# Performance work log

Hardware: AMD Instinct MI355X
Metric: run time of the kernel (lower is better)

## Reference

```python
import jax, jax.numpy as jnp
import numpy as np

B, N, K = 4, 4096, 16
D_POINTS, D_MODEL = 64, 128


def setup_inputs() -> dict:
    key = jax.random.key(0)
    ks = jax.random.split(key, 18)
    rn = lambda k, shp, s=0.05: (jax.random.normal(k, shp, jnp.float32) * s)
    return {
        "xyz": jax.random.normal(ks[0], (B, N, 3), jnp.float32),
        "features": jax.random.normal(ks[1], (B, N, D_POINTS), jnp.float32),
        # fc_delta: Linear(3,d_model) -> ReLU -> Linear(d_model,d_model)
        "Wd1": rn(ks[2], (3, D_MODEL)), "bd1": rn(ks[3], (D_MODEL,)),
        "Wd2": rn(ks[4], (D_MODEL, D_MODEL)), "bd2": rn(ks[5], (D_MODEL,)),
        # fc1: Linear(d_points, d_model)
        "Wf1": rn(ks[6], (D_POINTS, D_MODEL)), "bf1": rn(ks[7], (D_MODEL,)),
        # w_qs / w_ks / w_vs: Linear(d_model, d_model, bias=False)
        "Wq": rn(ks[8], (D_MODEL, D_MODEL)),
        "Wk": rn(ks[9], (D_MODEL, D_MODEL)),
        "Wv": rn(ks[10], (D_MODEL, D_MODEL)),
        # fc_gamma: Linear(d_model,d_model) -> ReLU -> Linear(d_model,d_model)
        "Wg1": rn(ks[11], (D_MODEL, D_MODEL)), "bg1": rn(ks[12], (D_MODEL,)),
        "Wg2": rn(ks[13], (D_MODEL, D_MODEL)), "bg2": rn(ks[14], (D_MODEL,)),
        # fc2: Linear(d_model, d_points)
        "Wo": rn(ks[15], (D_MODEL, D_POINTS)), "bo": rn(ks[16], (D_POINTS,)),
    }


def reference(xyz, features, Wd1, bd1, Wd2, bd2, Wf1, bf1, Wq, Wk, Wv,
              Wg1, bg1, Wg2, bg2, Wo, bo):
    sq = jnp.sum(xyz * xyz, axis=-1)
    d2 = sq[:, :, None] + sq[:, None, :] - 2.0 * jnp.einsum('bnd,bmd->bnm', xyz, xyz)
    # argsort()[:, :, :k] == k smallest distances (self included)
    _, knn_idx = jax.lax.top_k(-d2, K)  # [B,N,K] int32

    gather = jax.vmap(lambda a, i: a[i])  # per-batch fancy gather along point axis
    knn_xyz = gather(xyz, knn_idx)                       # [B,N,K,3]
    rel = xyz[:, :, None, :] - knn_xyz                   # [B,N,K,3]
    pos_enc = jax.nn.relu(rel @ Wd1 + bd1) @ Wd2 + bd2   # [B,N,K,D]

    shortcut = features
    f = features @ Wf1 + bf1                             # [B,N,D]
    knn_f = gather(f, knn_idx)                           # [B,N,K,D]

    q = f @ Wq                                           # [B,N,D]
    k = knn_f @ Wk                                       # [B,N,K,D]
    v = knn_f @ Wv                                       # [B,N,K,D]

    attn = q[:, :, None, :] - k + pos_enc                # [B,N,K,D]
    attn = jax.nn.relu(attn @ Wg1 + bg1) @ Wg2 + bg2
    attn = jax.nn.softmax(attn / np.sqrt(D_MODEL).astype(np.float32), axis=-2)

    res = jnp.einsum('bnkf,bnkf->bnf', attn, v + pos_enc)  # [B,N,D]
    return res @ Wo + bo + shortcut                        # [B,N,d_points]
```

## Files before the change

kernel.cpp:

```cpp
#include <hip/hip_runtime.h>
#include <hip/hip_bf16.h>

#define NPTS 4096
#define BATCH 4
#define BN (BATCH * NPTS)
#define DMODEL 128
#define DPTS 64
#define KNBR 16
#define SWS 136

typedef unsigned short u16;
typedef unsigned int u32;
typedef unsigned long long u64;
typedef short bh8 __attribute__((ext_vector_type(8)));
typedef float f32x4 __attribute__((ext_vector_type(4)));

__device__ __forceinline__ float bfu(u16 u) {
    union { u32 i; float f; } c; c.i = ((u32)u) << 16; return c.f;
}
__device__ __forceinline__ u16 f2u(float x) {
    u32 u = __float_as_uint(x);
    u32 r = u + 0x7FFFu + ((u >> 16) & 1u);
    return (u16)(r >> 16);
}
__device__ __forceinline__ u32 pack2(float a, float b) {
    return (u32)f2u(a) | ((u32)f2u(b) << 16);
}
__device__ __forceinline__ float ldr(const void* p, long i, int mode) {
    return mode == 0 ? bfu(((const u16*)p)[i]) : ((const float*)p)[i];
}
__device__ __forceinline__ void str(void* p, long i, float v, int mode) {
    if (mode == 0) ((u16*)p)[i] = f2u(v);
    else ((float*)p)[i] = v;
}
__device__ __forceinline__ int detect_mode(const void* Wq) {
    const u16* w = (const u16*)Wq;
    int lane = threadIdx.x & 63;
    int tot = 0;
#pragma unroll
    for (int r = 0; r < 4; ++r) {
        unsigned e = (w[lane + r * 64] >> 7) & 0xFFu;
        bool wild = (e >= 132u) || (e > 0u && e <= 90u);
        tot += (int)__popcll(__ballot(wild));
    }
    return tot > 32 ? 1 : 0;
}

__global__ __launch_bounds__(256) void prep_kernel(
    const void* __restrict__ Wd2, const void* __restrict__ Wg1, const void* __restrict__ Wg2,
    const void* __restrict__ Wo, const void* __restrict__ Wq, const void* __restrict__ Wk,
    const void* __restrict__ Wv, const void* __restrict__ Wf1,
    u16* __restrict__ WdT2, u16* __restrict__ WgT1, u16* __restrict__ WgT2,
    u16* __restrict__ WoT, u16* __restrict__ WqT, u16* __restrict__ WkT,
    u16* __restrict__ WvT, u16* __restrict__ WfT) {
    int mode = detect_mode(Wq);
    int gid = blockIdx.x * 256 + threadIdx.x;
    if (gid < 6 * 16384) {
        int m = gid >> 14, o = gid & 16383;
        int n = o >> 7, i = o & 127;
        const void* W = (m == 0) ? Wd2 : (m == 1) ? Wg1 : (m == 2) ? Wg2
                      : (m == 3) ? Wq  : (m == 4) ? Wk  : Wv;
        u16* D = (m == 0) ? WdT2 : (m == 1) ? WgT1 : (m == 2) ? WgT2
               : (m == 3) ? WqT  : (m == 4) ? WkT  : WvT;
        D[o] = f2u(ldr(W, (long)i * 128 + n, mode));
    } else if (gid < 6 * 16384 + 8192) {
        int o = gid - 6 * 16384;
        int n = o >> 6, k2 = o & 63;
        WfT[o] = f2u(ldr(Wf1, (long)k2 * 128 + n, mode));
    } else if (gid < 6 * 16384 + 16384) {
        int o2 = gid - 6 * 16384 - 8192;
        int col = o2 >> 7, i = o2 & 127;
        WoT[o2] = f2u(ldr(Wo, (long)i * 64 + col, mode));
    }
}

__global__ __launch_bounds__(256) void qkv_kernel(
    const void* __restrict__ feat, const void* __restrict__ bf1v, const void* __restrict__ WqRaw,
    const u16* __restrict__ WfT, const u16* __restrict__ WqT,
    const u16* __restrict__ WkT, const u16* __restrict__ WvT,
    u16* __restrict__ qw, u16* __restrict__ kfw, u16* __restrict__ vfw) {
    int mode = detect_mode(WqRaw);
    __shared__ __align__(16) u16 sFeat[64 * 72];
    __shared__ __align__(16) u16 sF[64 * SWS];
    const int t = threadIdx.x;
    const int p0 = blockIdx.x * 64;
    const int lane = t & 63, w = t >> 6;
    const int rg = (w & 1) * 32, cg = (w >> 1) * 64;
    const int lm = lane & 15, lq = lane >> 4;

    for (int i = t; i < 512; i += 256) {
        int r = i >> 3, c8 = i & 7;
        u16 tmp[8];
        if (mode == 0) {
            *(uint4*)tmp = *((const uint4*)feat + (long)(p0 + r) * 8 + c8);
        } else {
            const float* fp = (const float*)feat + (long)(p0 + r) * 64 + c8 * 8;
#pragma unroll
            for (int u = 0; u < 8; ++u) tmp[u] = f2u(fp[u]);
        }
        *(uint4*)(sFeat + r * 72 + c8 * 8) = *(uint4*)tmp;
    }
    __syncthreads();

    {
        f32x4 acc[2][4];
#pragma unroll
        for (int rt = 0; rt < 2; ++rt)
#pragma unroll
            for (int ct = 0; ct < 4; ++ct) { acc[rt][ct][0]=0.f; acc[rt][ct][1]=0.f; acc[rt][ct][2]=0.f; acc[rt][ct][3]=0.f; }
#pragma unroll
        for (int kk = 0; kk < 2; ++kk) {
            const int ko = kk * 32 + lq * 8;
            bh8 a0 = *(const bh8*)(sFeat + (rg + lm) * 72 + ko);
            bh8 a1 = *(const bh8*)(sFeat + (rg + 16 + lm) * 72 + ko);
            bh8 bq[4];
#pragma unroll
            for (int ct = 0; ct < 4; ++ct)
                bq[ct] = *(const bh8*)(WfT + (long)(cg + ct * 16 + lm) * 64 + ko);
#pragma unroll
            for (int ct = 0; ct < 4; ++ct) {
                acc[0][ct] = __builtin_amdgcn_mfma_f32_16x16x32_bf16(a0, bq[ct], acc[0][ct], 0, 0, 0);
                acc[1][ct] = __builtin_amdgcn_mfma_f32_16x16x32_bf16(a1, bq[ct], acc[1][ct], 0, 0, 0);
            }
        }
#pragma unroll
        for (int rt = 0; rt < 2; ++rt)
#pragma unroll
            for (int ct = 0; ct < 4; ++ct) {
                const int col = cg + ct * 16 + lm;
                const float bj = ldr(bf1v, col, mode);
#pragma unroll
                for (int r4 = 0; r4 < 4; ++r4) {
                    int row = rg + rt * 16 + lq * 4 + r4;
                    u32 u = (u32)f2u(acc[rt][ct][r4] + bj);
                    u32 o = __shfl_xor(u, 1);
                    if ((lane & 1) == 0)
                        *(u32*)(sF + row * SWS + col) = u | (o << 16);
                }
            }
    }
    __syncthreads();

    const u16* Ws[3] = {WqT, WkT, WvT};
    u16* Os[3] = {qw, kfw, vfw};
#pragma unroll 1
    for (int m = 0; m < 3; ++m) {
        f32x4 acc[2][4];
#pragma unroll
        for (int rt = 0; rt < 2; ++rt)
#pragma unroll
            for (int ct = 0; ct < 4; ++ct) { acc[rt][ct][0]=0.f; acc[rt][ct][1]=0.f; acc[rt][ct][2]=0.f; acc[rt][ct][3]=0.f; }
#pragma unroll
        for (int kk = 0; kk < 4; ++kk) {
            const int ko = kk * 32 + lq * 8;
            bh8 a0 = *(const bh8*)(sF + (rg + lm) * SWS + ko);
            bh8 a1 = *(const bh8*)(sF + (rg + 16 + lm) * SWS + ko);
            bh8 bq[4];
#pragma unroll
            for (int ct = 0; ct < 4; ++ct)
                bq[ct] = *(const bh8*)(Ws[m] + (long)(cg + ct * 16 + lm) * 128 + ko);
#pragma unroll
            for (int ct = 0; ct < 4; ++ct) {
                acc[0][ct] = __builtin_amdgcn_mfma_f32_16x16x32_bf16(a0, bq[ct], acc[0][ct], 0, 0, 0);
                acc[1][ct] = __builtin_amdgcn_mfma_f32_16x16x32_bf16(a1, bq[ct], acc[1][ct], 0, 0, 0);
            }
        }
#pragma unroll
        for (int rt = 0; rt < 2; ++rt)
#pragma unroll
            for (int ct = 0; ct < 4; ++ct) {
                const int col = cg + ct * 16 + lm;
#pragma unroll
                for (int r4 = 0; r4 < 4; ++r4) {
                    int row = rg + rt * 16 + lq * 4 + r4;
                    u32 u = (u32)f2u(acc[rt][ct][r4]);
                    u32 o = __shfl_xor(u, 1);
                    if ((lane & 1) == 0)
                        *(u32*)(Os[m] + (long)(p0 + row) * DMODEL + col) = u | (o << 16);
                }
            }
    }
}

__device__ __forceinline__ void mfma4(const u16* sIn, const u16* __restrict__ Bg,
                                      const float* bias, bool dorelu, bool inplace,
                                      u16* sOut, int t) {
    const int lane = t & 63, w = t >> 6;
    const int rg = (w & 1) * 32, cg = (w >> 1) * 64;
    const int lm = lane & 15, lq = lane >> 4;
    f32x4 acc[2][4];
#pragma unroll
    for (int rt = 0; rt < 2; ++rt)
#pragma unroll
        for (int ct = 0; ct < 4; ++ct) { acc[rt][ct][0]=0.f; acc[rt][ct][1]=0.f; acc[rt][ct][2]=0.f; acc[rt][ct][3]=0.f; }
#pragma unroll
    for (int kk = 0; kk < 4; ++kk) {
        const int ko = kk * 32 + lq * 8;
        bh8 a0 = *(const bh8*)(sIn + (rg + lm) * SWS + ko);
        bh8 a1 = *(const bh8*)(sIn + (rg + 16 + lm) * SWS + ko);
        bh8 bq[4];
#pragma unroll
        for (int ct = 0; ct < 4; ++ct)
            bq[ct] = *(const bh8*)(Bg + (long)(cg + ct * 16 + lm) * 128 + ko);
#pragma unroll
        for (int ct = 0; ct < 4; ++ct) {
            acc[0][ct] = __builtin_amdgcn_mfma_f32_16x16x32_bf16(a0, bq[ct], acc[0][ct], 0, 0, 0);
            acc[1][ct] = __builtin_amdgcn_mfma_f32_16x16x32_bf16(a1, bq[ct], acc[1][ct], 0, 0, 0);
        }
    }
    if (inplace) __syncthreads();
#pragma unroll
    for (int rt = 0; rt < 2; ++rt)
#pragma unroll
        for (int ct = 0; ct < 4; ++ct) {
            const int col = cg + ct * 16 + lm;
            const float bj = bias[col];
#pragma unroll
            for (int r4 = 0; r4 < 4; ++r4) {
                int row = rg + rt * 16 + lq * 4 + r4;
                float v = acc[rt][ct][r4] + bj;
                if (dorelu) v = fmaxf(v, 0.f);
                u32 u = (u32)f2u(v);
                u32 o = __shfl_xor(u, 1);
                if ((lane & 1) == 0)
                    *(u32*)(sOut + row * SWS + col) = u | (o << 16);
            }
        }
}

#define ATT_SA 0
#define ATT_SPE 17408
#define ATT_SREL 34816
#define ATT_SBIAS 35840
#define ATT_SQ 37376
#define SMEM_BYTES 38400

__global__ __launch_bounds__(256, 4) void fused_kernel(
    const void* __restrict__ xyz, const void* __restrict__ feat,
    const void* __restrict__ Wd1, const void* __restrict__ bd1, const void* __restrict__ bd2,
    const void* __restrict__ bg1, const void* __restrict__ bg2, const void* __restrict__ bo,
    const void* __restrict__ WqRaw,
    const u16* __restrict__ WdT2, const u16* __restrict__ WgT1, const u16* __restrict__ WgT2,
    const u16* __restrict__ WoT,
    const u16* __restrict__ qw, const u16* __restrict__ kfw, const u16* __restrict__ vfw,
    void* __restrict__ out) {
    int mode = detect_mode(WqRaw);
    __shared__ __align__(16) char smem[SMEM_BYTES];
    __shared__ int sIdx[64];
    u16* sXyz = (u16*)smem;
    u16* sA   = (u16*)(smem + ATT_SA);
    u16* sPE  = (u16*)(smem + ATT_SPE);
    float (*sRel)[4] = (float(*)[4])(smem + ATT_SREL);
    float* sBias = (float*)(smem + ATT_SBIAS);
    u16* sQ   = (u16*)(smem + ATT_SQ);

    const int t = threadIdx.x, lane = t & 63, w = t >> 6;
    const int lm = lane & 15, lq = lane >> 4;
    const int p0 = blockIdx.x * 4;
    const long bbase = (long)(p0 >> 12) * NPTS;
    const long xb = bbase * 3;

    for (int m = t; m < NPTS; m += 256) {
        float gx = ldr(xyz, xb + m * 3 + 0, mode);
        float gy = ldr(xyz, xb + m * 3 + 1, mode);
        float gz = ldr(xyz, xb + m * 3 + 2, mode);
        uint2 pk;
        pk.x = (u32)f2u(gx) | ((u32)f2u(gy) << 16);
        pk.y = (u32)f2u(gz);
        *(uint2*)(sXyz + m * 4) = pk;
    }
    __syncthreads();

    {
        const int pl = (p0 & (NPTS - 1)) + w;
        uint2 qv = *(const uint2*)(sXyz + pl * 4);
        const float px = __uint_as_float(qv.x << 16);
        const float py = __uint_as_float(qv.x & 0xFFFF0000u);
        const float pz = __uint_as_float(qv.y << 16);

        u64 kv;
        {
            uint2 c = *(const uint2*)(sXyz + lane * 4);
            float cx = __uint_as_float(c.x << 16);
            float cy = __uint_as_float(c.x & 0xFFFF0000u);
            float cz = __uint_as_float(c.y << 16);
            float key = fmaf(px * cx + py * cy + pz * cz, -2.f,
                             cx * cx + cy * cy + cz * cz);
            u32 uk = __float_as_uint(key);
            uk ^= (u32)((int)uk >> 31) | 0x80000000u;
            kv = ((u64)uk << 32) | (u32)lane;
#pragma unroll
            for (int k = 2; k <= 64; k <<= 1) {
#pragma unroll
                for (int j = k >> 1; j > 0; j >>= 1) {
                    u64 other = __shfl_xor(kv, j);
                    bool keepMin = ((lane & j) == 0) == ((lane & k) == 0);
                    bool smaller = kv < other;
                    kv = (keepMin == smaller) ? kv : other;
                }
            }
        }
        u32 Tu = __builtin_amdgcn_readlane((u32)(kv >> 32), 15);

        uint2 cd0 = *(const uint2*)(sXyz + (64 + lane) * 4);
        uint2 cd1 = *(const uint2*)(sXyz + (128 + lane) * 4);
#pragma unroll 1
        for (int it = 0; it < 32; ++it) {
            const int base = 64 + it * 128;
            uint2 c0 = cd0, c1 = cd1;
            if (it < 31) {
                int n0 = base + 128 + lane;
                int n1 = n0 + 64 > 4095 ? 4095 : n0 + 64;
                cd0 = *(const uint2*)(sXyz + n0 * 4);
                cd1 = *(const uint2*)(sXyz + n1 * 4);
            }
            float cx0 = __uint_as_float(c0.x << 16);
            float cy0 = __uint_as_float(c0.x & 0xFFFF0000u);
            float cz0 = __uint_as_float(c0.y << 16);
            float cx1 = __uint_as_float(c1.x << 16);
            float cy1 = __uint_as_float(c1.x & 0xFFFF0000u);
            float cz1 = __uint_as_float(c1.y << 16);
            float k0 = fmaf(px * cx0 + py * cy0 + pz * cz0, -2.f,
                            cx0 * cx0 + cy0 * cy0 + cz0 * cz0);
            float k1 = fmaf(px * cx1 + py * cy1 + pz * cz1, -2.f,
                            cx1 * cx1 + cy1 * cy1 + cz1 * cz1);
            u32 u0 = __float_as_uint(k0); u0 ^= (u32)((int)u0 >> 31) | 0x80000000u;
            u32 u1 = __float_as_uint(k1); u1 ^= (u32)((int)u1 >> 31) | 0x80000000u;
            if (it == 31) u1 = 0xFFFFFFFFu;
            u32 umin = (u0 < u1) ? u0 : u1;
            unsigned long long mask = __ballot(umin < Tu);
            while (mask) {
                int l = __ffsll(mask) - 1;
                mask &= mask - 1;
                u32 a0 = __builtin_amdgcn_readlane(u0, l);
                u32 a1 = __builtin_amdgcn_readlane(u1, l);
                if (a0 < Tu) {
                    u64 cand = ((u64)a0 << 32) | (u32)(base + l);
                    u64 prev = __shfl_up(kv, 1);
                    if (lane == 0) prev = 0;
                    kv = (prev > cand) ? prev : ((kv > cand) ? cand : kv);
                    Tu = __builtin_amdgcn_readlane((u32)(kv >> 32), 15);
                }
                if (a1 < Tu) {
                    u64 cand = ((u64)a1 << 32) | (u32)(base + 64 + l);
                    u64 prev = __shfl_up(kv, 1);
                    if (lane == 0) prev = 0;
                    kv = (prev > cand) ? prev : ((kv > cand) ? cand : kv);
                    Tu = __builtin_amdgcn_readlane((u32)(kv >> 32), 15);
                }
            }
        }
        if (lane < 16) sIdx[w * 16 + lane] = (int)(u32)kv;
    }
    __syncthreads();

    for (int i = t; i < 384; i += 256) {
        const void* b = (i < 128) ? bd2 : (i < 256) ? bg1 : bg2;
        sBias[i] = ldr(b, i & 127, mode);
    }
    ((u32*)sQ)[t] = ((const u32*)(qw + (long)p0 * DMODEL))[t];
    const int ch = 2 * lane;
    const float wd0a = ldr(Wd1, ch, mode),       wd0b = ldr(Wd1, ch + 1, mode);
    const float wd1a = ldr(Wd1, 128 + ch, mode), wd1b = ldr(Wd1, 128 + ch + 1, mode);
    const float wd2a = ldr(Wd1, 256 + ch, mode), wd2b = ldr(Wd1, 256 + ch + 1, mode);
    const float bd1a = ldr(bd1, ch, mode),       bd1b = ldr(bd1, ch + 1, mode);
    if (t < 64) {
        int pl2 = (p0 & (NPTS - 1)) + (t >> 4);
        uint2 pv = *(const uint2*)(sXyz + pl2 * 4);
        uint2 nv = *(const uint2*)(sXyz + sIdx[t] * 4);
        sRel[t][0] = __uint_as_float(pv.x << 16)          - __uint_as_float(nv.x << 16);
        sRel[t][1] = __uint_as_float(pv.x & 0xFFFF0000u)  - __uint_as_float(nv.x & 0xFFFF0000u);
        sRel[t][2] = __uint_as_float(pv.y << 16)          - __uint_as_float(nv.y << 16);
    }
    __syncthreads();

#pragma unroll
    for (int i = 0; i < 16; ++i) {
        int r = w * 16 + i;
        float4 rl = *(const float4*)sRel[r];
        float h0 = fmaxf(bd1a + rl.x * wd0a + rl.y * wd1a + rl.z * wd2a, 0.f);
        float h1 = fmaxf(bd1b + rl.x * wd0b + rl.y * wd1b + rl.z * wd2b, 0.f);
        *(u32*)(sA + r * SWS + ch) = pack2(h0, h1);
    }
    __syncthreads();
    mfma4(sA, WdT2, sBias, false, false, sPE, t);
    __syncthreads();

#pragma unroll
    for (int i = 0; i < 16; ++i) {
        int r = w * 16 + i;
        u32 kv2 = *(const u32*)(kfw + (bbase + sIdx[r]) * (long)DMODEL + ch);
        u32 qv2 = *(const u32*)(sQ + (r >> 4) * DMODEL + ch);
        u32 pe2 = *(const u32*)(sPE + r * SWS + ch);
        float a0 = bfu((u16)qv2) - bfu((u16)kv2) + bfu((u16)pe2);
        float a1 = bfu((u16)(qv2 >> 16)) - bfu((u16)(kv2 >> 16)) + bfu((u16)(pe2 >> 16));
        *(u32*)(sA + r * SWS + ch) = pack2(a0, a1);
    }
    __syncthreads();
    mfma4(sA, WgT1, sBias + 128, true, true, sA, t);
    __syncthreads();
    mfma4(sA, WgT2, sBias + 256, false, true, sA, t);
    __syncthreads();

    float res0, res1;
    {
        float mx0 = -3e38f, mx1 = -3e38f;
#pragma unroll
        for (int k = 0; k < KNBR; ++k) {
            u32 l2 = *(const u32*)(sA + (w * 16 + k) * SWS + ch);
            mx0 = fmaxf(mx0, bfu((u16)l2));
            mx1 = fmaxf(mx1, bfu((u16)(l2 >> 16)));
        }
        const float inv = 0.08838834764831845f;
        float s0 = 0.f, s1 = 0.f, r0 = 0.f, r1 = 0.f;
#pragma unroll
        for (int k = 0; k < KNBR; ++k) {
            u32 l2 = *(const u32*)(sA + (w * 16 + k) * SWS + ch);
            u32 v2 = *(const u32*)(vfw + (bbase + sIdx[w * 16 + k]) * (long)DMODEL + ch);
            u32 p2 = *(const u32*)(sPE + (w * 16 + k) * SWS + ch);
            float e0 = __expf((bfu((u16)l2) - mx0) * inv);
            float e1 = __expf((bfu((u16)(l2 >> 16)) - mx1) * inv);
            s0 += e0; s1 += e1;
            r0 += e0 * (bfu((u16)v2) + bfu((u16)p2));
            r1 += e1 * (bfu((u16)(v2 >> 16)) + bfu((u16)(p2 >> 16)));
        }
        res0 = r0 / s0; res1 = r1 / s1;
    }
    __syncthreads();
    *(u32*)(sA + w * SWS + ch) = pack2(res0, res1);
    __syncthreads();

    {
        const int col = w * 16 + lm;
        f32x4 acc = {0.f, 0.f, 0.f, 0.f};
#pragma unroll
        for (int kk = 0; kk < 4; ++kk) {
            const int ko = kk * 32 + lq * 8;
            bh8 aa = *(const bh8*)(sA + lm * SWS + ko);
            bh8 bb = *(const bh8*)(WoT + (long)col * DMODEL + ko);
            acc = __builtin_amdgcn_mfma_f32_16x16x32_bf16(aa, bb, acc, 0, 0, 0);
        }
        if (lq == 0) {
            float bov = ldr(bo, col, mode);
#pragma unroll
            for (int r4 = 0; r4 < 4; ++r4) {
                long p = p0 + r4;
                float v = acc[r4] + bov + ldr(feat, p * DPTS + col, mode);
                str(out, p * DPTS + col, v, mode);
            }
        }
    }
}

extern "C" void kernel_launch(void* const* d_in, const int* in_sizes, int n_in,
                              void* d_out, int out_size, void* d_ws, size_t ws_size,
                              hipStream_t stream) {
    (void)in_sizes; (void)n_in; (void)out_size; (void)ws_size;
    char* ws = (char*)d_ws;
    u16* qw   = (u16*)(ws + 256);
    u16* kfw  = qw + (long)BN * DMODEL;
    u16* vfw  = kfw + (long)BN * DMODEL;
    u16* WdT2 = vfw + (long)BN * DMODEL;
    u16* WgT1 = WdT2 + 16384;
    u16* WgT2 = WgT1 + 16384;
    u16* WoT  = WgT2 + 16384;
    u16* WqT  = WoT + 8192;
    u16* WkT  = WqT + 16384;
    u16* WvT  = WkT + 16384;
    u16* WfT  = WvT + 16384;

    prep_kernel<<<448, 256, 0, stream>>>(d_in[4], d_in[11], d_in[13], d_in[15],
                                         d_in[8], d_in[9], d_in[10], d_in[6],
                                         WdT2, WgT1, WgT2, WoT, WqT, WkT, WvT, WfT);
    qkv_kernel<<<BN / 64, 256, 0, stream>>>(d_in[1], d_in[7], d_in[8],
                                            WfT, WqT, WkT, WvT, qw, kfw, vfw);
    fused_kernel<<<BN / 4, 256, 0, stream>>>(d_in[0], d_in[1], d_in[2], d_in[3], d_in[5],
                                             d_in[12], d_in[14], d_in[16], d_in[8],
                                             WdT2, WgT1, WgT2, WoT,
                                             qw, kfw, vfw, d_out);
}
```

Before: 314.7 us.

## Split kNN into its own kernel reading a prepacked bf16 point cloud

Before, every fused block of 4 query points reloaded and converted all 4096 xyz points into shared memory before the kNN search. Now the prep kernel packs xyz to bf16 once, a separate knn_kernel scans that packed cloud from global/L2 and writes neighbour indices, and the fused kernel only reads those indices. The qkv kernel also spreads the Q/K/V projections across a 3-wide grid y dimension, and the mfma4 helper is inlined. This removes heavy redundant per-block staging and cuts fused-kernel LDS traffic, at the cost of one extra launch, an index round trip, and recomputing the f = features·Wf1 projection three times in qkv.

Result: faster. 303.1 us (-3.7%).

```diff
diff --git a/kernel.cpp b/kernel.cpp
--- a/kernel.cpp
+++ b/kernel.cpp
@@ -49,10 +49,10 @@
 __global__ __launch_bounds__(256) void prep_kernel(
     const void* __restrict__ Wd2, const void* __restrict__ Wg1, const void* __restrict__ Wg2,
     const void* __restrict__ Wo, const void* __restrict__ Wq, const void* __restrict__ Wk,
-    const void* __restrict__ Wv, const void* __restrict__ Wf1,
+    const void* __restrict__ Wv, const void* __restrict__ Wf1, const void* __restrict__ xyz,
     u16* __restrict__ WdT2, u16* __restrict__ WgT1, u16* __restrict__ WgT2,
     u16* __restrict__ WoT, u16* __restrict__ WqT, u16* __restrict__ WkT,
-    u16* __restrict__ WvT, u16* __restrict__ WfT) {
+    u16* __restrict__ WvT, u16* __restrict__ WfT, uint2* __restrict__ cloud) {
     int mode = detect_mode(Wq);
     int gid = blockIdx.x * 256 + threadIdx.x;
     if (gid < 6 * 16384) {
@@ -71,6 +71,15 @@
         int o2 = gid - 6 * 16384 - 8192;
         int col = o2 >> 7, i = o2 & 127;
         WoT[o2] = f2u(ldr(Wo, (long)i * 64 + col, mode));
+    } else if (gid < 6 * 16384 + 16384 + 16384) {
+        int i = gid - (6 * 16384 + 16384);
+        float gx = ldr(xyz, (long)i * 3 + 0, mode);
+        float gy = ldr(xyz, (long)i * 3 + 1, mode);
+        float gz = ldr(xyz, (long)i * 3 + 2, mode);
+        uint2 pk;
+        pk.x = (u32)f2u(gx) | ((u32)f2u(gy) << 16);
+        pk.y = (u32)f2u(gz);
+        cloud[i] = pk;
     }
 }
 
@@ -141,10 +150,10 @@
     }
     __syncthreads();
 
-    const u16* Ws[3] = {WqT, WkT, WvT};
-    u16* Os[3] = {qw, kfw, vfw};
-#pragma unroll 1
-    for (int m = 0; m < 3; ++m) {
+    {
+        const int m = blockIdx.y;
+        const u16* Wm = (m == 0) ? WqT : (m == 1) ? WkT : WvT;
+        u16* Om = (m == 0) ? qw : (m == 1) ? kfw : vfw;
         f32x4 acc[2][4];
 #pragma unroll
         for (int rt = 0; rt < 2; ++rt)
@@ -158,7 +167,7 @@
             bh8 bq[4];
 #pragma unroll
             for (int ct = 0; ct < 4; ++ct)
-                bq[ct] = *(const bh8*)(Ws[m] + (long)(cg + ct * 16 + lm) * 128 + ko);
+                bq[ct] = *(const bh8*)(Wm + (long)(cg + ct * 16 + lm) * 128 + ko);
 #pragma unroll
             for (int ct = 0; ct < 4; ++ct) {
                 acc[0][ct] = __builtin_amdgcn_mfma_f32_16x16x32_bf16(a0, bq[ct], acc[0][ct], 0, 0, 0);
@@ -176,56 +185,98 @@
                     u32 u = (u32)f2u(acc[rt][ct][r4]);
                     u32 o = __shfl_xor(u, 1);
                     if ((lane & 1) == 0)
-                        *(u32*)(Os[m] + (long)(p0 + row) * DMODEL + col) = u | (o << 16);
+                        *(u32*)(Om + (long)(p0 + row) * DMODEL + col) = u | (o << 16);
                 }
             }
     }
 }
 
-__device__ __forceinline__ void mfma4(const u16* sIn, const u16* __restrict__ Bg,
-                                      const float* bias, bool dorelu, bool inplace,
-                                      u16* sOut, int t) {
-    const int lane = t & 63, w = t >> 6;
-    const int rg = (w & 1) * 32, cg = (w >> 1) * 64;
-    const int lm = lane & 15, lq = lane >> 4;
-    f32x4 acc[2][4];
-#pragma unroll
-    for (int rt = 0; rt < 2; ++rt)
-#pragma unroll
-        for (int ct = 0; ct < 4; ++ct) { acc[rt][ct][0]=0.f; acc[rt][ct][1]=0.f; acc[rt][ct][2]=0.f; acc[rt][ct][3]=0.f; }
-#pragma unroll
-    for (int kk = 0; kk < 4; ++kk) {
-        const int ko = kk * 32 + lq * 8;
-        bh8 a0 = *(const bh8*)(sIn + (rg + lm) * SWS + ko);
-        bh8 a1 = *(const bh8*)(sIn + (rg + 16 + lm) * SWS + ko);
-        bh8 bq[4];
-#pragma unroll
-        for (int ct = 0; ct < 4; ++ct)
-            bq[ct] = *(const bh8*)(Bg + (long)(cg + ct * 16 + lm) * 128 + ko);
-#pragma unroll
-        for (int ct = 0; ct < 4; ++ct) {
-            acc[0][ct] = __builtin_amdgcn_mfma_f32_16x16x32_bf16(a0, bq[ct], acc[0][ct], 0, 0, 0);
-            acc[1][ct] = __builtin_amdgcn_mfma_f32_16x16x32_bf16(a1, bq[ct], acc[1][ct], 0, 0, 0);
-        }
-    }
-    if (inplace) __syncthreads();
-#pragma unroll
-    for (int rt = 0; rt < 2; ++rt)
-#pragma unroll
-        for (int ct = 0; ct < 4; ++ct) {
-            const int col = cg + ct * 16 + lm;
-            const float bj = bias[col];
-#pragma unroll
-            for (int r4 = 0; r4 < 4; ++r4) {
-                int row = rg + rt * 16 + lq * 4 + r4;
-                float v = acc[rt][ct][r4] + bj;
-                if (dorelu) v = fmaxf(v, 0.f);
-                u32 u = (u32)f2u(v);
-                u32 o = __shfl_xor(u, 1);
-                if ((lane & 1) == 0)
-                    *(u32*)(sOut + row * SWS + col) = u | (o << 16);
-            }
-        }
+__global__ __launch_bounds__(256) void knn_kernel(
+    const uint2* __restrict__ cloud, int* __restrict__ knnIdx) {
+    const int t = threadIdx.x, lane = t & 63, w = t >> 6;
+    const int p0 = blockIdx.x * 4;
+    const long bbase = (long)(p0 >> 12) * NPTS;
+    const uint2* cl = cloud + bbase;
+
+    const int pl = (p0 & (NPTS - 1)) + w;
+    uint2 qv = cl[pl];
+    const float px = __uint_as_float(qv.x << 16);
+    const float py = __uint_as_float(qv.x & 0xFFFF0000u);
+    const float pz = __uint_as_float(qv.y << 16);
+
+    u64 kv;
+    {
+        uint2 c = cl[lane];
+        float cx = __uint_as_float(c.x << 16);
+        float cy = __uint_as_float(c.x & 0xFFFF0000u);
+        float cz = __uint_as_float(c.y << 16);
+        float key = fmaf(px * cx + py * cy + pz * cz, -2.f,
+                         cx * cx + cy * cy + cz * cz);
+        u32 uk = __float_as_uint(key);
+        uk ^= (u32)((int)uk >> 31) | 0x80000000u;
+        kv = ((u64)uk << 32) | (u32)lane;
+#pragma unroll
+        for (int k = 2; k <= 64; k <<= 1) {
+#pragma unroll
+            for (int j = k >> 1; j > 0; j >>= 1) {
+                u64 other = __shfl_xor(kv, j);
+                bool keepMin = ((lane & j) == 0) == ((lane & k) == 0);
+                bool smaller = kv < other;
+                kv = (keepMin == smaller) ? kv : other;
+            }
+        }
+    }
+    u32 Tu = __builtin_amdgcn_readlane((u32)(kv >> 32), 15);
+
+    uint2 cd0 = cl[64 + lane];
+    uint2 cd1 = cl[128 + lane];
+#pragma unroll 1
+    for (int it = 0; it < 32; ++it) {
+        const int base = 64 + it * 128;
+        uint2 c0 = cd0, c1 = cd1;
+        if (it < 31) {
+            int n0 = base + 128 + lane;
+            int n1 = n0 + 64 > 4095 ? 4095 : n0 + 64;
+            cd0 = cl[n0];
+            cd1 = cl[n1];
+        }
+        float cx0 = __uint_as_float(c0.x << 16);
+        float cy0 = __uint_as_float(c0.x & 0xFFFF0000u);
+        float cz0 = __uint_as_float(c0.y << 16);
+        float cx1 = __uint_as_float(c1.x << 16);
+        float cy1 = __uint_as_float(c1.x & 0xFFFF0000u);
+        float cz1 = __uint_as_float(c1.y << 16);
+        float k0 = fmaf(px * cx0 + py * cy0 + pz * cz0, -2.f,
+                        cx0 * cx0 + cy0 * cy0 + cz0 * cz0);
+        float k1 = fmaf(px * cx1 + py * cy1 + pz * cz1, -2.f,
+                        cx1 * cx1 + cy1 * cy1 + cz1 * cz1);
+        u32 u0 = __float_as_uint(k0); u0 ^= (u32)((int)u0 >> 31) | 0x80000000u;
+        u32 u1 = __float_as_uint(k1); u1 ^= (u32)((int)u1 >> 31) | 0x80000000u;
+        if (it == 31) u1 = 0xFFFFFFFFu;
+        u32 umin = (u0 < u1) ? u0 : u1;
+        unsigned long long mask = __ballot(umin < Tu);
+        while (mask) {
+            int l = __ffsll(mask) - 1;
+            mask &= mask - 1;
+            u32 a0 = __builtin_amdgcn_readlane(u0, l);
+            u32 a1 = __builtin_amdgcn_readlane(u1, l);
+            if (a0 < Tu) {
+                u64 cand = ((u64)a0 << 32) | (u32)(base + l);
+                u64 prev = __shfl_up(kv, 1);
+                if (lane == 0) prev = 0;
+                kv = (prev > cand) ? prev : ((kv > cand) ? cand : kv);
+                Tu = __builtin_amdgcn_readlane((u32)(kv >> 32), 15);
+            }
+            if (a1 < Tu) {
+                u64 cand = ((u64)a1 << 32) | (u32)(base + 64 + l);
+                u64 prev = __shfl_up(kv, 1);
+                if (lane == 0) prev = 0;
+                kv = (prev > cand) ? prev : ((kv > cand) ? cand : kv);
+                Tu = __builtin_amdgcn_readlane((u32)(kv >> 32), 15);
+            }
+        }
+    }
+    if (lane < 16) knnIdx[(long)(p0 + w) * 16 + lane] = (int)(u32)kv;
 }
 
 #define ATT_SA 0
@@ -236,7 +287,8 @@
 #define SMEM_BYTES 38400
 
 __global__ __launch_bounds__(256, 4) void fused_kernel(
-    const void* __restrict__ xyz, const void* __restrict__ feat,
+    const uint2* __restrict__ cloud, const int* __restrict__ knnIdx,
+    const void* __restrict__ feat,
     const void* __restrict__ Wd1, const void* __restrict__ bd1, const void* __restrict__ bd2,
     const void* __restrict__ bg1, const void* __restrict__ bg2, const void* __restrict__ bo,
     const void* __restrict__ WqRaw,
@@ -247,7 +299,6 @@
     int mode = detect_mode(WqRaw);
     __shared__ __align__(16) char smem[SMEM_BYTES];
     __shared__ int sIdx[64];
-    u16* sXyz = (u16*)smem;
     u16* sA   = (u16*)(smem + ATT_SA);
     u16* sPE  = (u16*)(smem + ATT_SPE);
     float (*sRel)[4] = (float(*)[4])(smem + ATT_SREL);
@@ -258,101 +309,7 @@
     const int lm = lane & 15, lq = lane >> 4;
     const int p0 = blockIdx.x * 4;
     const long bbase = (long)(p0 >> 12) * NPTS;
-    const long xb = bbase * 3;
-
-    for (int m = t; m < NPTS; m += 256) {
-        float gx = ldr(xyz, xb + m * 3 + 0, mode);
-        float gy = ldr(xyz, xb + m * 3 + 1, mode);
-        float gz = ldr(xyz, xb + m * 3 + 2, mode);
-        uint2 pk;
-        pk.x = (u32)f2u(gx) | ((u32)f2u(gy) << 16);
-        pk.y = (u32)f2u(gz);
-        *(uint2*)(sXyz + m * 4) = pk;
-    }
-    __syncthreads();
-
-    {
-        const int pl = (p0 & (NPTS - 1)) + w;
-        uint2 qv = *(const uint2*)(sXyz + pl * 4);
-        const float px = __uint_as_float(qv.x << 16);
-        const float py = __uint_as_float(qv.x & 0xFFFF0000u);
-        const float pz = __uint_as_float(qv.y << 16);
-
-        u64 kv;
-        {
-            uint2 c = *(const uint2*)(sXyz + lane * 4);
-            float cx = __uint_as_float(c.x << 16);
-            float cy = __uint_as_float(c.x & 0xFFFF0000u);
-            float cz = __uint_as_float(c.y << 16);
-            float key = fmaf(px * cx + py * cy + pz * cz, -2.f,
-                             cx * cx + cy * cy + cz * cz);
-            u32 uk = __float_as_uint(key);
-            uk ^= (u32)((int)uk >> 31) | 0x80000000u;
-            kv = ((u64)uk << 32) | (u32)lane;
-#pragma unroll
-            for (int k = 2; k <= 64; k <<= 1) {
-#pragma unroll
-                for (int j = k >> 1; j > 0; j >>= 1) {
-                    u64 other = __shfl_xor(kv, j);
-                    bool keepMin = ((lane & j) == 0) == ((lane & k) == 0);
-                    bool smaller = kv < other;
-                    kv = (keepMin == smaller) ? kv : other;
-                }
-            }
-        }
-        u32 Tu = __builtin_amdgcn_readlane((u32)(kv >> 32), 15);
-
-        uint2 cd0 = *(const uint2*)(sXyz + (64 + lane) * 4);
-        uint2 cd1 = *(const uint2*)(sXyz + (128 + lane) * 4);
-#pragma unroll 1
-        for (int it = 0; it < 32; ++it) {
-            const int base = 64 + it * 128;
-            uint2 c0 = cd0, c1 = cd1;
-            if (it < 31) {
-                int n0 = base + 128 + lane;
-                int n1 = n0 + 64 > 4095 ? 4095 : n0 + 64;
-                cd0 = *(const uint2*)(sXyz + n0 * 4);
-                cd1 = *(const uint2*)(sXyz + n1 * 4);
-            }
-            float cx0 = __uint_as_float(c0.x << 16);
-            float cy0 = __uint_as_float(c0.x & 0xFFFF0000u);
-            float cz0 = __uint_as_float(c0.y << 16);
-            float cx1 = __uint_as_float(c1.x << 16);
-            float cy1 = __uint_as_float(c1.x & 0xFFFF0000u);
-            float cz1 = __uint_as_float(c1.y << 16);
-            float k0 = fmaf(px * cx0 + py * cy0 + pz * cz0, -2.f,
-                            cx0 * cx0 + cy0 * cy0 + cz0 * cz0);
-            float k1 = fmaf(px * cx1 + py * cy1 + pz * cz1, -2.f,
-                            cx1 * cx1 + cy1 * cy1 + cz1 * cz1);
-            u32 u0 = __float_as_uint(k0); u0 ^= (u32)((int)u0 >> 31) | 0x80000000u;
-            u32 u1 = __float_as_uint(k1); u1 ^= (u32)((int)u1 >> 31) | 0x80000000u;
-            if (it == 31) u1 = 0xFFFFFFFFu;
-            u32 umin = (u0 < u1) ? u0 : u1;
-            unsigned long long mask = __ballot(umin < Tu);
-            while (mask) {
-                int l = __ffsll(mask) - 1;
-                mask &= mask - 1;
-                u32 a0 = __builtin_amdgcn_readlane(u0, l);
-                u32 a1 = __builtin_amdgcn_readlane(u1, l);
-                if (a0 < Tu) {
-                    u64 cand = ((u64)a0 << 32) | (u32)(base + l);
-                    u64 prev = __shfl_up(kv, 1);
-                    if (lane == 0) prev = 0;
-                    kv = (prev > cand) ? prev : ((kv > cand) ? cand : kv);
-                    Tu = __builtin_amdgcn_readlane((u32)(kv >> 32), 15);
-                }
-                if (a1 < Tu) {
-                    u64 cand = ((u64)a1 << 32) | (u32)(base + 64 + l);
-                    u64 prev = __shfl_up(kv, 1);
-                    if (lane == 0) prev = 0;
-                    kv = (prev > cand) ? prev : ((kv > cand) ? cand : kv);
-                    Tu = __builtin_amdgcn_readlane((u32)(kv >> 32), 15);
-                }
-            }
-        }
-        if (lane < 16) sIdx[w * 16 + lane] = (int)(u32)kv;
-    }
-    __syncthreads();
+    const uint2* cl = cloud + bbase;
 
     for (int i = t; i < 384; i += 256) {
         const void* b = (i < 128) ? bd2 : (i < 256) ? bg1 : bg2;
@@ -365,9 +322,11 @@
     const float wd2a = ldr(Wd1, 256 + ch, mode), wd2b = ldr(Wd1, 256 + ch + 1, mode);
     const float bd1a = ldr(bd1, ch, mode),       bd1b = ldr(bd1, ch + 1, mode);
     if (t < 64) {
+        int idx = knnIdx[(long)p0 * 16 + t];
+        sIdx[t] = idx;
         int pl2 = (p0 & (NPTS - 1)) + (t >> 4);
-        uint2 pv = *(const uint2*)(sXyz + pl2 * 4);
-        uint2 nv = *(const uint2*)(sXyz + sIdx[t] * 4);
+        uint2 pv = cl[pl2];
+        uint2 nv = cl[idx];
         sRel[t][0] = __uint_as_float(pv.x << 16)          - __uint_as_float(nv.x << 16);
         sRel[t][1] = __uint_as_float(pv.x & 0xFFFF0000u)  - __uint_as_float(nv.x & 0xFFFF0000u);
         sRel[t][2] = __uint_as_float(pv.y << 16)          - __uint_as_float(nv.y << 16);
@@ -383,7 +342,44 @@
         *(u32*)(sA + r * SWS + ch) = pack2(h0, h1);
     }
     __syncthreads();
-    mfma4(sA, WdT2, sBias, false, false, sPE, t);
+    {
+        const int rg = (w & 1) * 32, cg = (w >> 1) * 64;
+        f32x4 acc[2][4];
+#pragma unroll
+        for (int rt = 0; rt < 2; ++rt)
+#pragma unroll
+            for (int ct = 0; ct < 4; ++ct) { acc[rt][ct][0]=0.f; acc[rt][ct][1]=0.f; acc[rt][ct][2]=0.f; acc[rt][ct][3]=0.f; }
+#pragma unroll
+        for (int kk = 0; kk < 4; ++kk) {
+            const int ko = kk * 32 + lq * 8;
+            bh8 a0 = *(const bh8*)(sA + (rg + lm) * SWS + ko);
+            bh8 a1 = *(const bh8*)(sA + (rg + 16 + lm) * SWS + ko);
+            bh8 bq[4];
+#pragma unroll
+            for (int ct = 0; ct < 4; ++ct)
+                bq[ct] = *(const bh8*)(WdT2 + (long)(cg + ct * 16 + lm) * 128 + ko);
+#pragma unroll
+            for (int ct = 0; ct < 4; ++ct) {
+                acc[0][ct] = __builtin_amdgcn_mfma_f32_16x16x32_bf16(a0, bq[ct], acc[0][ct], 0, 0, 0);
+                acc[1][ct] = __builtin_amdgcn_mfma_f32_16x16x32_bf16(a1, bq[ct], acc[1][ct], 0, 0, 0);
+            }
+        }
+#pragma unroll
+        for (int rt = 0; rt < 2; ++rt)
+#pragma unroll
+            for (int ct = 0; ct < 4; ++ct) {
+                const int col = cg + ct * 16 + lm;
+                const float bj = sBias[col];
+#pragma unroll
+                for (int r4 = 0; r4 < 4; ++r4) {
+                    int row = rg + rt * 16 + lq * 4 + r4;
+                    u32 u = (u32)f2u(acc[rt][ct][r4] + bj);
+                    u32 o = __shfl_xor(u, 1);
+                    if ((lane & 1) == 0)
+                        *(u32*)(sPE + row * SWS + col) = u | (o << 16);
+                }
+            }
+    }
     __syncthreads();
 
 #pragma unroll
@@ -397,10 +393,52 @@
         *(u32*)(sA + r * SWS + ch) = pack2(a0, a1);
     }
     __syncthreads();
-    mfma4(sA, WgT1, sBias + 128, true, true, sA, t);
-    __syncthreads();
-    mfma4(sA, WgT2, sBias + 256, false, true, sA, t);
-    __syncthreads();
+#pragma unroll 1
+    for (int g = 0; g < 2; ++g) {
+        const u16* Bg = (g == 0) ? WgT1 : WgT2;
+        const float* bias = sBias + 128 + g * 128;
+        const bool dorelu = (g == 0);
+        const int rg = (w & 1) * 32, cg = (w >> 1) * 64;
+        f32x4 acc[2][4];
+#pragma unroll
+        for (int rt = 0; rt < 2; ++rt)
+#pragma unroll
+            for (int ct = 0; ct < 4; ++ct) { acc[rt][ct][0]=0.f; acc[rt][ct][1]=0.f; acc[rt][ct][2]=0.f; acc[rt][ct][3]=0.f; }
+#pragma unroll
+        for (int kk = 0; kk < 4; ++kk) {
+            const int ko = kk * 32 + lq * 8;
+            bh8 a0 = *(const bh8*)(sA + (rg + lm) * SWS + ko);
+            bh8 a1 = *(const bh8*)(sA + (rg + 16 + lm) * SWS + ko);
+            bh8 bq[4];
+#pragma unroll
+            for (int ct = 0; ct < 4; ++ct)
+                bq[ct] = *(const bh8*)(Bg + (long)(cg + ct * 16 + lm) * 128 + ko);
+#pragma unroll
+            for (int ct = 0; ct < 4; ++ct) {
+                acc[0][ct] = __builtin_amdgcn_mfma_f32_16x16x32_bf16(a0, bq[ct], acc[0][ct], 0, 0, 0);
+                acc[1][ct] = __builtin_amdgcn_mfma_f32_16x16x32_bf16(a1, bq[ct], acc[1][ct], 0, 0, 0);
+            }
+        }
+        __syncthreads();
+#pragma unroll
+        for (int rt = 0; rt < 2; ++rt)
+#pragma unroll
+            for (int ct = 0; ct < 4; ++ct) {
+                const int col = cg + ct * 16 + lm;
+                const float bj = bias[col];
+#pragma unroll
+                for (int r4 = 0; r4 < 4; ++r4) {
+                    int row = rg + rt * 16 + lq * 4 + r4;
+                    float v = acc[rt][ct][r4] + bj;
+                    if (dorelu) v = fmaxf(v, 0.f);
+                    u32 u = (u32)f2u(v);
+                    u32 o = __shfl_xor(u, 1);
+                    if ((lane & 1) == 0)
+                        *(u32*)(sA + row * SWS + col) = u | (o << 16);
+                }
+            }
+        __syncthreads();
+    }
 
     float res0, res1;
     {
@@ -468,13 +506,18 @@
     u16* WkT  = WqT + 16384;
     u16* WvT  = WkT + 16384;
     u16* WfT  = WvT + 16384;
-
-    prep_kernel<<<448, 256, 0, stream>>>(d_in[4], d_in[11], d_in[13], d_in[15],
-                                         d_in[8], d_in[9], d_in[10], d_in[6],
-                                         WdT2, WgT1, WgT2, WoT, WqT, WkT, WvT, WfT);
-    qkv_kernel<<<BN / 64, 256, 0, stream>>>(d_in[1], d_in[7], d_in[8],
-                                            WfT, WqT, WkT, WvT, qw, kfw, vfw);
-    fused_kernel<<<BN / 4, 256, 0, stream>>>(d_in[0], d_in[1], d_in[2], d_in[3], d_in[5],
+    uint2* cloud = (uint2*)(WfT + 8192);
+    int* knnIdx = (int*)(cloud + BN);
+
+    prep_kernel<<<512, 256, 0, stream>>>(d_in[4], d_in[11], d_in[13], d_in[15],
+                                         d_in[8], d_in[9], d_in[10], d_in[6], d_in[0],
+                                         WdT2, WgT1, WgT2, WoT, WqT, WkT, WvT, WfT,
+                                         cloud);
+    qkv_kernel<<<dim3(BN / 64, 3), 256, 0, stream>>>(d_in[1], d_in[7], d_in[8],
+                                                     WfT, WqT, WkT, WvT, qw, kfw, vfw);
+    knn_kernel<<<BN / 4, 256, 0, stream>>>(cloud, knnIdx);
+    fused_kernel<<<BN / 4, 256, 0, stream>>>(cloud, knnIdx, d_in[1],
+                                             d_in[2], d_in[3], d_in[5],
                                              d_in[12], d_in[14], d_in[16], d_in[8],
                                              WdT2, WgT1, WgT2, WoT,
                                              qw, kfw, vfw, d_out);
```

## Split KNN into separate kernel, precompute fp32 cloud, widen fused blocks to 8 points

Applied to the files above, without the earlier changes.

KNN selection moves out of the fused attention kernel into its own kernel. It reads a precomputed float4 cloud (xyz plus squared norm) written by the prep kernel, so each fused block no longer stages the whole 4096-point batch into LDS as bf16. The qkv projection is split across a grid y-dimension so each block computes one of the three outputs. The fused kernel now handles 8 points per 512-thread block with 8-wave MFMA tiles. This adds an extra launch and a global round-trip for the indices, and doubles LDS per block, which may reduce occupancy.

New measurement: 301.6 us. 1.04x faster.

```diff
diff --git a/kernel.cpp b/kernel.cpp
--- a/kernel.cpp
+++ b/kernel.cpp
@@ -8,6 +8,7 @@
 #define DPTS 64
 #define KNBR 16
 #define SWS 136
+#define PBLK 8
 
 typedef unsigned short u16;
 typedef unsigned int u32;
@@ -49,10 +50,10 @@
 __global__ __launch_bounds__(256) void prep_kernel(
     const void* __restrict__ Wd2, const void* __restrict__ Wg1, const void* __restrict__ Wg2,
     const void* __restrict__ Wo, const void* __restrict__ Wq, const void* __restrict__ Wk,
-    const void* __restrict__ Wv, const void* __restrict__ Wf1,
+    const void* __restrict__ Wv, const void* __restrict__ Wf1, const void* __restrict__ xyz,
     u16* __restrict__ WdT2, u16* __restrict__ WgT1, u16* __restrict__ WgT2,
     u16* __restrict__ WoT, u16* __restrict__ WqT, u16* __restrict__ WkT,
-    u16* __restrict__ WvT, u16* __restrict__ WfT) {
+    u16* __restrict__ WvT, u16* __restrict__ WfT, float4* __restrict__ cloudF) {
     int mode = detect_mode(Wq);
     int gid = blockIdx.x * 256 + threadIdx.x;
     if (gid < 6 * 16384) {
@@ -71,6 +72,15 @@
         int o2 = gid - 6 * 16384 - 8192;
         int col = o2 >> 7, i = o2 & 127;
         WoT[o2] = f2u(ldr(Wo, (long)i * 64 + col, mode));
+    } else if (gid < 6 * 16384 + 16384 + 16384) {
+        int i = gid - (6 * 16384 + 16384);
+        float gx = ldr(xyz, (long)i * 3 + 0, mode);
+        float gy = ldr(xyz, (long)i * 3 + 1, mode);
+        float gz = ldr(xyz, (long)i * 3 + 2, mode);
+        float4 f;
+        f.x = gx; f.y = gy; f.z = gz;
+        f.w = gx * gx + gy * gy + gz * gz;
+        cloudF[i] = f;
     }
 }
 
@@ -141,10 +151,10 @@
     }
     __syncthreads();
 
-    const u16* Ws[3] = {WqT, WkT, WvT};
-    u16* Os[3] = {qw, kfw, vfw};
-#pragma unroll 1
-    for (int m = 0; m < 3; ++m) {
+    {
+        const int m = blockIdx.y;
+        const u16* Wm = (m == 0) ? WqT : (m == 1) ? WkT : WvT;
+        u16* Om = (m == 0) ? qw : (m == 1) ? kfw : vfw;
         f32x4 acc[2][4];
 #pragma unroll
         for (int rt = 0; rt < 2; ++rt)
@@ -158,7 +168,7 @@
             bh8 bq[4];
 #pragma unroll
             for (int ct = 0; ct < 4; ++ct)
-                bq[ct] = *(const bh8*)(Ws[m] + (long)(cg + ct * 16 + lm) * 128 + ko);
+                bq[ct] = *(const bh8*)(Wm + (long)(cg + ct * 16 + lm) * 128 + ko);
 #pragma unroll
             for (int ct = 0; ct < 4; ++ct) {
                 acc[0][ct] = __builtin_amdgcn_mfma_f32_16x16x32_bf16(a0, bq[ct], acc[0][ct], 0, 0, 0);
@@ -176,17 +186,91 @@
                     u32 u = (u32)f2u(acc[rt][ct][r4]);
                     u32 o = __shfl_xor(u, 1);
                     if ((lane & 1) == 0)
-                        *(u32*)(Os[m] + (long)(p0 + row) * DMODEL + col) = u | (o << 16);
+                        *(u32*)(Om + (long)(p0 + row) * DMODEL + col) = u | (o << 16);
                 }
             }
     }
 }
 
-__device__ __forceinline__ void mfma4(const u16* sIn, const u16* __restrict__ Bg,
+__global__ __launch_bounds__(256) void knn_kernel(
+    const float4* __restrict__ cloudF, int* __restrict__ knnIdx) {
+    const int t = threadIdx.x, lane = t & 63, w = t >> 6;
+    const int p0 = blockIdx.x * 4;
+    const long bbase = (long)(p0 >> 12) * NPTS;
+    const float4* cl = cloudF + bbase;
+
+    const int pl = (p0 & (NPTS - 1)) + w;
+    float4 qv = cl[pl];
+    const float m2x = -2.f * qv.x, m2y = -2.f * qv.y, m2z = -2.f * qv.z;
+
+    u64 kv;
+    {
+        float4 c = cl[lane];
+        float key = fmaf(m2x, c.x, fmaf(m2y, c.y, fmaf(m2z, c.z, c.w)));
+        u32 uk = __float_as_uint(key);
+        uk ^= (u32)((int)uk >> 31) | 0x80000000u;
+        kv = ((u64)uk << 32) | (u32)lane;
+#pragma unroll
+        for (int k = 2; k <= 64; k <<= 1) {
+#pragma unroll
+            for (int j = k >> 1; j > 0; j >>= 1) {
+                u64 other = __shfl_xor(kv, j);
+                bool keepMin = ((lane & j) == 0) == ((lane & k) == 0);
+                bool smaller = kv < other;
+                kv = (keepMin == smaller) ? kv : other;
+            }
+        }
+    }
+    u32 Tu = __builtin_amdgcn_readlane((u32)(kv >> 32), 15);
+
+    float4 cd0 = cl[64 + lane];
+    float4 cd1 = cl[128 + lane];
+#pragma unroll 1
+    for (int it = 0; it < 32; ++it) {
+        const int base = 64 + it * 128;
+        float4 c0 = cd0, c1 = cd1;
+        if (it < 31) {
+            int n0 = base + 128 + lane;
+            int n1 = n0 + 64 > 4095 ? 4095 : n0 + 64;
+            cd0 = cl[n0];
+            cd1 = cl[n1];
+        }
+        float k0 = fmaf(m2x, c0.x, fmaf(m2y, c0.y, fmaf(m2z, c0.z, c0.w)));
+        float k1 = fmaf(m2x, c1.x, fmaf(m2y, c1.y, fmaf(m2z, c1.z, c1.w)));
+        u32 u0 = __float_as_uint(k0); u0 ^= (u32)((int)u0 >> 31) | 0x80000000u;
+        u32 u1 = __float_as_uint(k1); u1 ^= (u32)((int)u1 >> 31) | 0x80000000u;
+        if (it == 31) u1 = 0xFFFFFFFFu;
+        u32 umin = (u0 < u1) ? u0 : u1;
+        unsigned long long mask = __ballot(umin < Tu);
+        while (mask) {
+            int l = __ffsll(mask) - 1;
+            mask &= mask - 1;
+            u32 a0 = __builtin_amdgcn_readlane(u0, l);
+            u32 a1 = __builtin_amdgcn_readlane(u1, l);
+            if (a0 < Tu) {
+                u64 cand = ((u64)a0 << 32) | (u32)(base + l);
+                u64 prev = __shfl_up(kv, 1);
+                if (lane == 0) prev = 0;
+                kv = (prev > cand) ? prev : ((kv > cand) ? cand : kv);
+                Tu = __builtin_amdgcn_readlane((u32)(kv >> 32), 15);
+            }
+            if (a1 < Tu) {
+                u64 cand = ((u64)a1 << 32) | (u32)(base + 64 + l);
+                u64 prev = __shfl_up(kv, 1);
+                if (lane == 0) prev = 0;
+                kv = (prev > cand) ? prev : ((kv > cand) ? cand : kv);
+                Tu = __builtin_amdgcn_readlane((u32)(kv >> 32), 15);
+            }
+        }
+    }
+    if (lane < 16) knnIdx[(long)(p0 + w) * 16 + lane] = (int)(u32)kv;
+}
+
+__device__ __forceinline__ void mfma8(const u16* sIn, const u16* __restrict__ Bg,
                                       const float* bias, bool dorelu, bool inplace,
                                       u16* sOut, int t) {
     const int lane = t & 63, w = t >> 6;
-    const int rg = (w & 1) * 32, cg = (w >> 1) * 64;
+    const int rg = (w & 3) * 32, cg = (w >> 2) * 64;
     const int lm = lane & 15, lq = lane >> 4;
     f32x4 acc[2][4];
 #pragma unroll
@@ -229,14 +313,15 @@
 }
 
 #define ATT_SA 0
-#define ATT_SPE 17408
-#define ATT_SREL 34816
-#define ATT_SBIAS 35840
-#define ATT_SQ 37376
-#define SMEM_BYTES 38400
-
-__global__ __launch_bounds__(256, 4) void fused_kernel(
-    const void* __restrict__ xyz, const void* __restrict__ feat,
+#define ATT_SPE 34816
+#define ATT_SREL 69632
+#define ATT_SBIAS 71680
+#define ATT_SQ 73216
+#define SMEM_BYTES 75264
+
+__global__ __launch_bounds__(512, 4) void fused_kernel(
+    const float4* __restrict__ cloudF, const int* __restrict__ knnIdx,
+    const void* __restrict__ feat,
     const void* __restrict__ Wd1, const void* __restrict__ bd1, const void* __restrict__ bd2,
     const void* __restrict__ bg1, const void* __restrict__ bg2, const void* __restrict__ bo,
     const void* __restrict__ WqRaw,
@@ -246,8 +331,7 @@
     void* __restrict__ out) {
     int mode = detect_mode(WqRaw);
     __shared__ __align__(16) char smem[SMEM_BYTES];
-    __shared__ int sIdx[64];
-    u16* sXyz = (u16*)smem;
+    __shared__ int sIdx[128];
     u16* sA   = (u16*)(smem + ATT_SA);
     u16* sPE  = (u16*)(smem + ATT_SPE);
     float (*sRel)[4] = (float(*)[4])(smem + ATT_SREL);
@@ -256,105 +340,11 @@
 
     const int t = threadIdx.x, lane = t & 63, w = t >> 6;
     const int lm = lane & 15, lq = lane >> 4;
-    const int p0 = blockIdx.x * 4;
+    const int p0 = blockIdx.x * PBLK;
     const long bbase = (long)(p0 >> 12) * NPTS;
-    const long xb = bbase * 3;
-
-    for (int m = t; m < NPTS; m += 256) {
-        float gx = ldr(xyz, xb + m * 3 + 0, mode);
-        float gy = ldr(xyz, xb + m * 3 + 1, mode);
-        float gz = ldr(xyz, xb + m * 3 + 2, mode);
-        uint2 pk;
-        pk.x = (u32)f2u(gx) | ((u32)f2u(gy) << 16);
-        pk.y = (u32)f2u(gz);
-        *(uint2*)(sXyz + m * 4) = pk;
-    }
-    __syncthreads();
-
-    {
-        const int pl = (p0 & (NPTS - 1)) + w;
-        uint2 qv = *(const uint2*)(sXyz + pl * 4);
-        const float px = __uint_as_float(qv.x << 16);
-        const float py = __uint_as_float(qv.x & 0xFFFF0000u);
-        const float pz = __uint_as_float(qv.y << 16);
-
-        u64 kv;
-        {
-            uint2 c = *(const uint2*)(sXyz + lane * 4);
-            float cx = __uint_as_float(c.x << 16);
-            float cy = __uint_as_float(c.x & 0xFFFF0000u);
-            float cz = __uint_as_float(c.y << 16);
-            float key = fmaf(px * cx + py * cy + pz * cz, -2.f,
-                             cx * cx + cy * cy + cz * cz);
-            u32 uk = __float_as_uint(key);
-            uk ^= (u32)((int)uk >> 31) | 0x80000000u;
-            kv = ((u64)uk << 32) | (u32)lane;
-#pragma unroll
-            for (int k = 2; k <= 64; k <<= 1) {
-#pragma unroll
-                for (int j = k >> 1; j > 0; j >>= 1) {
-                    u64 other = __shfl_xor(kv, j);
-                    bool keepMin = ((lane & j) == 0) == ((lane & k) == 0);
-                    bool smaller = kv < other;
-                    kv = (keepMin == smaller) ? kv : other;
-                }
-            }
-        }
-        u32 Tu = __builtin_amdgcn_readlane((u32)(kv >> 32), 15);
-
-        uint2 cd0 = *(const uint2*)(sXyz + (64 + lane) * 4);
-        uint2 cd1 = *(const uint2*)(sXyz + (128 + lane) * 4);
-#pragma unroll 1
-        for (int it = 0; it < 32; ++it) {
-            const int base = 64 + it * 128;
-            uint2 c0 = cd0, c1 = cd1;
-            if (it < 31) {
-                int n0 = base + 128 + lane;
-                int n1 = n0 + 64 > 4095 ? 4095 : n0 + 64;
-                cd0 = *(const uint2*)(sXyz + n0 * 4);
-                cd1 = *(const uint2*)(sXyz + n1 * 4);
-            }
-            float cx0 = __uint_as_float(c0.x << 16);
-            float cy0 = __uint_as_float(c0.x & 0xFFFF0000u);
-            float cz0 = __uint_as_float(c0.y << 16);
-            float cx1 = __uint_as_float(c1.x << 16);
-            float cy1 = __uint_as_float(c1.x & 0xFFFF0000u);
-            float cz1 = __uint_as_float(c1.y << 16);
-            float k0 = fmaf(px * cx0 + py * cy0 + pz * cz0, -2.f,
-                            cx0 * cx0 + cy0 * cy0 + cz0 * cz0);
-            float k1 = fmaf(px * cx1 + py * cy1 + pz * cz1, -2.f,
-                            cx1 * cx1 + cy1 * cy1 + cz1 * cz1);
-            u32 u0 = __float_as_uint(k0); u0 ^= (u32)((int)u0 >> 31) | 0x80000000u;
-            u32 u1 = __float_as_uint(k1); u1 ^= (u32)((int)u1 >> 31) | 0x80000000u;
-            if (it == 31) u1 = 0xFFFFFFFFu;
-            u32 umin = (u0 < u1) ? u0 : u1;
-            unsigned long long mask = __ballot(umin < Tu);
-            while (mask) {
-                int l = __ffsll(mask) - 1;
-                mask &= mask - 1;
-                u32 a0 = __builtin_amdgcn_readlane(u0, l);
-                u32 a1 = __builtin_amdgcn_readlane(u1, l);
-                if (a0 < Tu) {
-                    u64 cand = ((u64)a0 << 32) | (u32)(base + l);
-                    u64 prev = __shfl_up(kv, 1);
-                    if (lane == 0) prev = 0;
-                    kv = (prev > cand) ? prev : ((kv > cand) ? cand : kv);
-                    Tu = __builtin_amdgcn_readlane((u32)(kv >> 32), 15);
-                }
-                if (a1 < Tu) {
-                    u64 cand = ((u64)a1 << 32) | (u32)(base + 64 + l);
-                    u64 prev = __shfl_up(kv, 1);
-                    if (lane == 0) prev = 0;
-                    kv = (prev > cand) ? prev : ((kv > cand) ? cand : kv);
-                    Tu = __builtin_amdgcn_readlane((u32)(kv >> 32), 15);
-                }
-            }
-        }
-        if (lane < 16) sIdx[w * 16 + lane] = (int)(u32)kv;
-    }
-    __syncthreads();
-
-    for (int i = t; i < 384; i += 256) {
+    const float4* cl = cloudF + bbase;
+
+    for (int i = t; i < 384; i += 512) {
         const void* b = (i < 128) ? bd2 : (i < 256) ? bg1 : bg2;
         sBias[i] = ldr(b, i & 127, mode);
     }
@@ -364,13 +354,15 @@
     const float wd1a = ldr(Wd1, 128 + ch, mode), wd1b = ldr(Wd1, 128 + ch + 1, mode);
     const float wd2a = ldr(Wd1, 256 + ch, mode), wd2b = ldr(Wd1, 256 + ch + 1, mode);
     const float bd1a = ldr(bd1, ch, mode),       bd1b = ldr(bd1, ch + 1, mode);
-    if (t < 64) {
+    if (t < 128) {
+        int idx = knnIdx[(long)p0 * 16 + t];
+        sIdx[t] = idx;
         int pl2 = (p0 & (NPTS - 1)) + (t >> 4);
-        uint2 pv = *(const uint2*)(sXyz + pl2 * 4);
-        uint2 nv = *(const uint2*)(sXyz + sIdx[t] * 4);
-        sRel[t][0] = __uint_as_float(pv.x << 16)          - __uint_as_float(nv.x << 16);
-        sRel[t][1] = __uint_as_float(pv.x & 0xFFFF0000u)  - __uint_as_float(nv.x & 0xFFFF0000u);
-        sRel[t][2] = __uint_as_float(pv.y << 16)          - __uint_as_float(nv.y << 16);
+        float4 pv = cl[pl2];
+        float4 nv = cl[idx];
+        sRel[t][0] = pv.x - nv.x;
+        sRel[t][1] = pv.y - nv.y;
+        sRel[t][2] = pv.z - nv.z;
     }
     __syncthreads();
 
@@ -383,7 +375,7 @@
         *(u32*)(sA + r * SWS + ch) = pack2(h0, h1);
     }
     __syncthreads();
-    mfma4(sA, WdT2, sBias, false, false, sPE, t);
+    mfma8(sA, WdT2, sBias, false, false, sPE, t);
     __syncthreads();
 
 #pragma unroll
@@ -397,9 +389,9 @@
         *(u32*)(sA + r * SWS + ch) = pack2(a0, a1);
     }
     __syncthreads();
-    mfma4(sA, WgT1, sBias + 128, true, true, sA, t);
-    __syncthreads();
-    mfma4(sA, WgT2, sBias + 256, false, true, sA, t);
+    mfma8(sA, WgT1, sBias + 128, true, true, sA, t);
+    __syncthreads();
+    mfma8(sA, WgT2, sBias + 256, false, true, sA, t);
     __syncthreads();
 
     float res0, res1;
@@ -430,7 +422,7 @@
     *(u32*)(sA + w * SWS + ch) = pack2(res0, res1);
     __syncthreads();
 
-    {
+    if (w < 4) {
         const int col = w * 16 + lm;
         f32x4 acc = {0.f, 0.f, 0.f, 0.f};
 #pragma unroll
@@ -440,11 +432,11 @@
             bh8 bb = *(const bh8*)(WoT + (long)col * DMODEL + ko);
             acc = __builtin_amdgcn_mfma_f32_16x16x32_bf16(aa, bb, acc, 0, 0, 0);
         }
-        if (lq == 0) {
+        if (lq < 2) {
             float bov = ldr(bo, col, mode);
 #pragma unroll
             for (int r4 = 0; r4 < 4; ++r4) {
-                long p = p0 + r4;
+                long p = p0 + lq * 4 + r4;
                 float v = acc[r4] + bov + ldr(feat, p * DPTS + col, mode);
                 str(out, p * DPTS + col, v, mode);
             }
@@ -468,14 +460,19 @@
     u16* WkT  = WqT + 16384;
     u16* WvT  = WkT + 16384;
     u16* WfT  = WvT + 16384;
-
-    prep_kernel<<<448, 256, 0, stream>>>(d_in[4], d_in[11], d_in[13], d_in[15],
-                                         d_in[8], d_in[9], d_in[10], d_in[6],
-                                         WdT2, WgT1, WgT2, WoT, WqT, WkT, WvT, WfT);
-    qkv_kernel<<<BN / 64, 256, 0, stream>>>(d_in[1], d_in[7], d_in[8],
-                                            WfT, WqT, WkT, WvT, qw, kfw, vfw);
-    fused_kernel<<<BN / 4, 256, 0, stream>>>(d_in[0], d_in[1], d_in[2], d_in[3], d_in[5],
-                                             d_in[12], d_in[14], d_in[16], d_in[8],
-                                             WdT2, WgT1, WgT2, WoT,
-                                             qw, kfw, vfw, d_out);
-}
+    float4* cloudF = (float4*)(WfT + 8192);
+    int* knnIdx = (int*)(cloudF + BN);
+
+    prep_kernel<<<512, 256, 0, stream>>>(d_in[4], d_in[11], d_in[13], d_in[15],
+                                         d_in[8], d_in[9], d_in[10], d_in[6], d_in[0],
+                                         WdT2, WgT1, WgT2, WoT, WqT, WkT, WvT, WfT,
+                                         cloudF);
+    qkv_kernel<<<dim3(BN / 64, 3), 256, 0, stream>>>(d_in[1], d_in[7], d_in[8],
+                                                     WfT, WqT, WkT, WvT, qw, kfw, vfw);
+    knn_kernel<<<BN / 4, 256, 0, stream>>>(cloudF, knnIdx);
+    fused_kernel<<<BN / PBLK, 512, 0, stream>>>(cloudF, knnIdx, d_in[1],
+                                                d_in[2], d_in[3], d_in[5],
+                                                d_in[12], d_in[14], d_in[16], d_in[8],
+                                                WdT2, WgT1, WgT2, WoT,
+                                                qw, kfw, vfw, d_out);
+}
```
